# Kernel optimization log

Measured on AMD Instinct MI355X. Metric: run time of the kernel, lower is better.

Reference implementation:

```python
import jax, jax.numpy as jnp
import numpy as np

SIGMAS = [0.5, 1.0, 2.0, 4.0, 8.0]
FILTER_SIZE = int(4 * SIGMAS[-1] + 1)  # 33
PAD = int(2 * SIGMAS[-1])              # 16
K1, K2 = 0.01, 0.03
ALPHA = 0.025
COMPENSATION = 20.0
DATA_RANGE = 1.0


def _gauss_2d(size, sigma):
    coords = np.arange(size, dtype=np.float32) - size // 2
    g = np.exp(-coords ** 2 / (2.0 * sigma ** 2))
    g = g / g.sum()
    return np.outer(g, g)


def _build_g_masks():
    # [n_sigmas, 1, 33, 33] OIHW
    masks = np.stack([_gauss_2d(FILTER_SIZE, s)[None] for s in SIGMAS], axis=0)
    return jnp.asarray(masks, dtype=jnp.float32)


def setup_inputs() -> dict:
    key = jax.random.key(0)
    kx, ky = jax.random.split(key)
    x = jax.random.uniform(kx, (16, 1, 512, 512), dtype=jnp.float32)
    y = jax.random.uniform(ky, (16, 1, 512, 512), dtype=jnp.float32)
    return {"x": x, "y": y, "g_masks": _build_g_masks()}


def _conv(t, w):
    # t: [B,1,H,W], w: [O,1,33,33] -> [B,O,H,W] ('same' padding)
    return jax.lax.conv_general_dilated(
        t, w, window_strides=(1, 1), padding=[(PAD, PAD), (PAD, PAD)],
        dimension_numbers=("NCHW", "OIHW", "NCHW"))


def reference(x, y, g_masks):
    C1 = (K1 * DATA_RANGE) ** 2
    C2 = (K2 * DATA_RANGE) ** 2

    mux = _conv(x, g_masks)   # [B,5,H,W]
    muy = _conv(y, g_masks)
    mux2 = mux * mux
    muy2 = muy * muy
    muxy = mux * muy
    sigmax2 = _conv(x * x, g_masks) - mux2
    sigmay2 = _conv(y * y, g_masks) - muy2
    sigmaxy = _conv(x * y, g_masks) - muxy

    luminance = (2.0 * muxy + C1) / (mux2 + muy2 + C1)
    cs = (2.0 * sigmaxy + C2) / (sigmax2 + sigmay2 + C2)

    lM = luminance[:, -1, :, :]          # largest-scale luminance
    PIcs = jnp.prod(cs, axis=1)          # product of contrast-structure over scales
    loss_ms_ssim = 1.0 - lM * PIcs       # [B,H,W]

    loss_l1 = jnp.abs(x - y)             # [B,1,H,W]
    gaussian_l1 = _conv(loss_l1, g_masks[-1:]).mean(axis=1)  # [B,H,W]

    loss_mix = ALPHA * loss_ms_ssim + (1.0 - ALPHA) * gaussian_l1 / DATA_RANGE
    return (COMPENSATION * loss_mix).mean()
```

## Files before the change

kernel.cpp:

```cpp
#include <hip/hip_runtime.h>
#include <hip/hip_bf16.h>

namespace {

constexpr float kAlpha = 0.025f;
constexpr float kC1 = 1.0e-4f;
constexpr float kC2 = 9.0e-4f;

constexpr int MPS = 72;
constexpr int HTS = 72;

typedef __attribute__((ext_vector_type(8))) short short8;
typedef __attribute__((ext_vector_type(4))) float f32x4;

struct __align__(16) Smem {
  union {
    short mp[2][64 * MPS];
    short hbT[4][32 * HTS];
  };
  short l1T[32 * HTS];
  float red[4];
  int gtab[2][5][48];
};

union Frag {
  int i[4];
  int4 i4;
  short8 s8;
};

__device__ __forceinline__ unsigned f2bf(float f) {
  unsigned u = __float_as_uint(f);
  return (u + 0x7FFFu + ((u >> 16) & 1u)) >> 16;
}
__device__ __forceinline__ unsigned pk(float a, float b) {
  union {
    __hip_bfloat162 h;
    unsigned u;
  } c;
  c.h = __float22bfloat162_rn(make_float2(a, b));
  return c.u;
}
__device__ __forceinline__ float bfl(unsigned u) {
  return __uint_as_float(u << 16);
}
__device__ __forceinline__ float bfh(unsigned u) {
  return __uint_as_float(u & 0xFFFF0000u);
}
__device__ __forceinline__ float frcp(float x) {
  return __builtin_amdgcn_rcpf(x);
}

__device__ __forceinline__ short8 wbuild2(const int* tb, int nt, int kt) {
  Frag u;
#pragma unroll
  for (int j = 0; j < 4; ++j) u.i[j] = tb[16 * kt - 8 * nt + 8 + j];
  return u.s8;
}

__device__ __forceinline__ void load_xy(const Smem& sm, int row, int quad,
                                        Frag fx[2], Frag fy[2]) {
  const short* px = &sm.mp[0][row * MPS + quad * 8];
  const short* py = &sm.mp[1][row * MPS + quad * 8];
  fx[0].i4 = *(const int4*)(px);
  fx[1].i4 = *(const int4*)(px + 32);
  fy[0].i4 = *(const int4*)(py);
  fy[1].i4 = *(const int4*)(py + 32);
}

template <bool USE_WS>
__global__ __launch_bounds__(256, 4) void msssim_l1_kernel(
    const float* __restrict__ x, const float* __restrict__ y,
    const float* __restrict__ gm, float* __restrict__ partial,
    float* __restrict__ out) {
  __shared__ Smem sm;
  const int tid = threadIdx.x;
  const int lane = tid & 63;
  const int w = tid >> 6;
  const int quad = lane >> 4;
  const int l16 = lane & 15;
  const f32x4 kZ = {0.f, 0.f, 0.f, 0.f};

  float corr;
  {
    float traw4 = (lane < 33) ? gm[4 * 1089 + 528 + lane] : 0.f;
    float g = traw4 * rsqrtf(__shfl(traw4, 16, 64));
    float se = g, st = bfl(f2bf(g));
#pragma unroll
    for (int off = 32; off > 0; off >>= 1) {
      se += __shfl_xor(se, off, 64);
      st += __shfl_xor(st, off, 64);
    }
    float r1 = se / st;
    corr = r1 * r1;
  }

  {
    int* gt = &sm.gtab[0][0][0];
    for (int q = tid; q < 480; q += 256) {
      int par = q >= 240;
      int rem = par ? q - 240 : q;
      int s = rem / 48;
      int i = rem - s * 48;
      int t0 = 2 * i + par;
      const float* grow = gm + s * 1089 + 528;
      float rsc = rsqrtf(grow[16]);
      int g0 = t0 - 31, g1 = t0 - 30;
      unsigned lo = (g0 >= 0 && g0 <= 32) ? f2bf(grow[g0] * rsc) : 0u;
      unsigned hi = (g1 >= 0 && g1 <= 32) ? f2bf(grow[g1] * rsc) : 0u;
      gt[q] = (int)(lo | (hi << 16));
    }
  }

  const int D = (quad * 8 - l16 + 31) >> 1;
  const int* gD = &sm.gtab[(l16 & 1) ? 0 : 1][0][0] + D - 8;

  const float* xb = x + blockIdx.z * (512 * 512);
  const float* yb = y + blockIdx.z * (512 * 512);
  const int rb = blockIdx.y * 32 - 16;
  const int cb = blockIdx.x * 32 - 16;
  for (int f = tid; f < 1024; f += 256) {
    int pr = f >> 4;
    int pc = (f & 15) << 2;
    int gr = rb + pr, gc = cb + pc;
    float4 vx = make_float4(0.f, 0.f, 0.f, 0.f);
    float4 vy = vx;
    if (gr >= 0 && gr < 512 && gc >= 0 && gc < 512) {
      vx = *(const float4*)(xb + gr * 512 + gc);
      vy = *(const float4*)(yb + gr * 512 + gc);
    }
    const int base = pr * MPS + pc;
    *(int2*)(&sm.mp[0][base]) =
        make_int2((int)pk(vx.x, vx.y), (int)pk(vx.z, vx.w));
    *(int2*)(&sm.mp[1][base]) =
        make_int2((int)pk(vy.x, vy.y), (int)pk(vy.z, vy.w));
  }
  __syncthreads();

  Frag A[4][2];
  Frag dA[2];
#pragma unroll
  for (int mt = 0; mt < 4; ++mt) {
    Frag fx[2], fy[2];
    load_xy(sm, mt * 16 + l16, quad, fx, fy);
    if (mt == w) {
#pragma unroll
      for (int h = 0; h < 2; ++h)
#pragma unroll
        for (int i = 0; i < 4; ++i) {
          unsigned ux = (unsigned)fx[h].i[i], uy = (unsigned)fy[h].i[i];
          dA[h].i[i] =
              (int)pk(fabsf(bfl(ux) - bfl(uy)), fabsf(bfh(ux) - bfh(uy)));
        }
    }
    if (w == 0) {
      A[mt][0] = fx[0];
      A[mt][1] = fx[1];
    } else if (w == 1) {
      A[mt][0] = fy[0];
      A[mt][1] = fy[1];
    } else {
#pragma unroll
      for (int h = 0; h < 2; ++h)
#pragma unroll
        for (int i = 0; i < 4; ++i) {
          unsigned ux = (unsigned)fx[h].i[i], uy = (unsigned)fy[h].i[i];
          float xl = bfl(ux), xh = bfh(ux), yl = bfl(uy), yh = bfh(uy);
          A[mt][h].i[i] = (w == 2) ? (int)pk(fmaf(xl, xl, yl * yl),
                                            fmaf(xh, xh, yh * yh))
                                   : (int)pk(xl * yl, xh * yh);
        }
    }
  }

  {
    const int* tb = gD + 4 * 48;
#pragma unroll
    for (int nt = 0; nt < 2; ++nt) {
      short8 w0 = wbuild2(tb, nt, 0);
      short8 w1 = wbuild2(tb, nt, 1);
      f32x4 acc = __builtin_amdgcn_mfma_f32_16x16x32_bf16(dA[0].s8, w0, kZ, 0,
                                                          0, 0);
      acc = __builtin_amdgcn_mfma_f32_16x16x32_bf16(dA[1].s8, w1, acc, 0, 0,
                                                    0);
      *(int2*)(&sm.l1T[(nt * 16 + l16) * HTS + w * 16 + quad * 4]) =
          make_int2((int)pk(acc[0], acc[1]), (int)pk(acc[2], acc[3]));
    }
  }
  __syncthreads();

  const int mtv = w >> 1, ntv = w & 1;
  f32x4 Pcs = {1.f, 1.f, 1.f, 1.f};
  f32x4 lumP = {0.f, 0.f, 0.f, 0.f};
  f32x4 l1v = {0.f, 0.f, 0.f, 0.f};

#pragma unroll
  for (int s = 0; s < 5; ++s) {
    const int* tb = gD + s * 48;
#pragma unroll
    for (int nt = 0; nt < 2; ++nt) {
      short8 w0 = wbuild2(tb, nt, 0);
      short8 w1 = wbuild2(tb, nt, 1);
#pragma unroll
      for (int mt = 0; mt < 4; ++mt) {
        f32x4 acc = __builtin_amdgcn_mfma_f32_16x16x32_bf16(A[mt][0].s8, w0,
                                                            kZ, 0, 0, 0);
        acc = __builtin_amdgcn_mfma_f32_16x16x32_bf16(A[mt][1].s8, w1, acc, 0,
                                                      0, 0);
        *(int2*)(&sm.hbT[w][(nt * 16 + l16) * HTS + mt * 16 + quad * 4]) =
            make_int2((int)pk(acc[0], acc[1]), (int)pk(acc[2], acc[3]));
      }
    }
    __syncthreads();

    short8 wa0 = wbuild2(tb, mtv, 0);
    short8 wa1 = wbuild2(tb, mtv, 1);
    f32x4 mux, muy, T;
#pragma unroll
    for (int m = 0; m < 4; ++m) {
      const short* bp = &sm.hbT[m][(ntv * 16 + l16) * HTS + quad * 8];
      Frag b0, b1;
      b0.i4 = *(const int4*)(bp);
      b1.i4 = *(const int4*)(bp + 32);
      f32x4 acc =
          __builtin_amdgcn_mfma_f32_16x16x32_bf16(wa0, b0.s8, kZ, 0, 0, 0);
      acc = __builtin_amdgcn_mfma_f32_16x16x32_bf16(wa1, b1.s8, acc, 0, 0, 0);
      if (m == 0) {
        mux = acc;
      } else if (m == 1) {
        muy = acc;
      } else if (m == 2) {
#pragma unroll
        for (int r = 0; r < 4; ++r)
          T[r] = (acc[r] - mux[r] * mux[r]) - muy[r] * muy[r];
      } else {
#pragma unroll
        for (int r = 0; r < 4; ++r) {
          float cs =
              (2.f * (acc[r] - mux[r] * muy[r]) + kC2) * frcp(T[r] + kC2);
          Pcs[r] *= cs;
          if (s == 4)
            lumP[r] = ((2.f * (mux[r] * muy[r]) + kC1) *
                       frcp((mux[r] * mux[r] + muy[r] * muy[r]) + kC1)) *
                      Pcs[r];
        }
      }
    }
    if (s == 4) {
      const short* lp = &sm.l1T[(ntv * 16 + l16) * HTS + quad * 8];
      Frag c0, c1;
      c0.i4 = *(const int4*)(lp);
      c1.i4 = *(const int4*)(lp + 32);
      f32x4 a2 =
          __builtin_amdgcn_mfma_f32_16x16x32_bf16(wa0, c0.s8, kZ, 0, 0, 0);
      a2 = __builtin_amdgcn_mfma_f32_16x16x32_bf16(wa1, c1.s8, a2, 0, 0, 0);
#pragma unroll
      for (int r = 0; r < 4; ++r) l1v[r] = a2[r] * corr;
    }
    __syncthreads();
  }

  float lsum = 0.f;
#pragma unroll
  for (int r = 0; r < 4; ++r)
    lsum += kAlpha * (1.f - lumP[r]) + (1.f - kAlpha) * l1v[r];
#pragma unroll
  for (int off = 32; off > 0; off >>= 1) lsum += __shfl_down(lsum, off, 64);
  if ((tid & 63) == 0) sm.red[tid >> 6] = lsum;
  __syncthreads();
  if (tid == 0) {
    float t = sm.red[0] + sm.red[1] + sm.red[2] + sm.red[3];
    if (USE_WS) {
      partial[blockIdx.x + (blockIdx.y << 4) + (blockIdx.z << 8)] = t;
    } else {
      atomicAdd(out, t * (20.f / (16.f * 512.f * 512.f)));
    }
  }
}

__global__ __launch_bounds__(256) void msssim_reduce_kernel(
    const float* __restrict__ partial, float* __restrict__ out) {
  const int tid = threadIdx.x;
  float s = 0.f;
#pragma unroll
  for (int i = 0; i < 16; ++i) s += partial[tid + (i << 8)];
#pragma unroll
  for (int off = 32; off > 0; off >>= 1) s += __shfl_xor(s, off, 64);
  __shared__ float red[4];
  if ((tid & 63) == 0) red[tid >> 6] = s;
  __syncthreads();
  if (tid == 0)
    out[0] =
        (red[0] + red[1] + red[2] + red[3]) * (20.f / (16.f * 512.f * 512.f));
}

}

extern "C" void kernel_launch(void* const* d_in, const int* in_sizes, int n_in,
                              void* d_out, int out_size, void* d_ws,
                              size_t ws_size, hipStream_t stream) {
  (void)in_sizes;
  (void)n_in;
  (void)out_size;
  const float* x = (const float*)d_in[0];
  const float* y = (const float*)d_in[1];
  const float* gm = (const float*)d_in[2];
  float* out = (float*)d_out;
  dim3 grid(16, 16, 16);
  if (d_ws != nullptr && ws_size >= 4096 * sizeof(float)) {
    float* partial = (float*)d_ws;
    msssim_l1_kernel<true>
        <<<grid, dim3(256), 0, stream>>>(x, y, gm, partial, out);
    msssim_reduce_kernel<<<1, dim3(256), 0, stream>>>(partial, out);
  } else {
    hipMemsetAsync(out, 0, sizeof(float), stream);
    msssim_l1_kernel<false>
        <<<grid, dim3(256), 0, stream>>>(x, y, gm, nullptr, out);
  }
}
```

Measured before the change: 126.0 us.

## Precompute x²+y² and xy planes in shared memory during tile load

The tile load now computes x²+y² and x·y in fp32 from the global loads and stores them as two extra bf16 planes in shared memory. Each wave then loads its A operand straight from its own plane, with no per-wave branching or per-fragment recompute. The shared row stride changes from 72 to 66 shorts to keep the union size down and alter bank mapping, so the 16-byte reads become pairs of 8-byte reads. The shared footprint grows, which could lower occupancy. The product terms are now formed from fp32 inputs rather than bf16-rounded ones, which changes numerics slightly.

```diff
diff --git a/kernel.cpp b/kernel.cpp
--- a/kernel.cpp
+++ b/kernel.cpp
@@ -7,7 +7,7 @@
 constexpr float kC1 = 1.0e-4f;
 constexpr float kC2 = 9.0e-4f;
 
-constexpr int MPS = 72;
+constexpr int MPS = 66;
 constexpr int HTS = 72;
 
 typedef __attribute__((ext_vector_type(8))) short short8;
@@ -15,7 +15,7 @@
 
 struct __align__(16) Smem {
   union {
-    short mp[2][64 * MPS];
+    short mp[4][64 * MPS];
     short hbT[4][32 * HTS];
   };
   short l1T[32 * HTS];
@@ -56,16 +56,6 @@
 #pragma unroll
   for (int j = 0; j < 4; ++j) u.i[j] = tb[16 * kt - 8 * nt + 8 + j];
   return u.s8;
-}
-
-__device__ __forceinline__ void load_xy(const Smem& sm, int row, int quad,
-                                        Frag fx[2], Frag fy[2]) {
-  const short* px = &sm.mp[0][row * MPS + quad * 8];
-  const short* py = &sm.mp[1][row * MPS + quad * 8];
-  fx[0].i4 = *(const int4*)(px);
-  fx[1].i4 = *(const int4*)(px + 32);
-  fy[0].i4 = *(const int4*)(py);
-  fy[1].i4 = *(const int4*)(py + 32);
 }
 
 template <bool USE_WS>
@@ -134,6 +124,14 @@
         make_int2((int)pk(vx.x, vx.y), (int)pk(vx.z, vx.w));
     *(int2*)(&sm.mp[1][base]) =
         make_int2((int)pk(vy.x, vy.y), (int)pk(vy.z, vy.w));
+    float s0 = fmaf(vx.x, vx.x, vy.x * vy.x);
+    float s1 = fmaf(vx.y, vx.y, vy.y * vy.y);
+    float s2 = fmaf(vx.z, vx.z, vy.z * vy.z);
+    float s3 = fmaf(vx.w, vx.w, vy.w * vy.w);
+    *(int2*)(&sm.mp[2][base]) = make_int2((int)pk(s0, s1), (int)pk(s2, s3));
+    *(int2*)(&sm.mp[3][base]) =
+        make_int2((int)pk(vx.x * vy.x, vx.y * vy.y),
+                  (int)pk(vx.z * vy.z, vx.w * vy.w));
   }
   __syncthreads();
 
@@ -141,36 +139,33 @@
   Frag dA[2];
 #pragma unroll
   for (int mt = 0; mt < 4; ++mt) {
+    const short* pa = &sm.mp[w][(mt * 16 + l16) * MPS + quad * 8];
+    *(int2*)&A[mt][0].i[0] = *(const int2*)(pa);
+    *(int2*)&A[mt][0].i[2] = *(const int2*)(pa + 4);
+    *(int2*)&A[mt][1].i[0] = *(const int2*)(pa + 32);
+    *(int2*)&A[mt][1].i[2] = *(const int2*)(pa + 36);
+  }
+  {
+    const int row = (w * 16 + l16) * MPS + quad * 8;
+    const short* px = &sm.mp[0][row];
+    const short* py = &sm.mp[1][row];
     Frag fx[2], fy[2];
-    load_xy(sm, mt * 16 + l16, quad, fx, fy);
-    if (mt == w) {
-#pragma unroll
-      for (int h = 0; h < 2; ++h)
-#pragma unroll
-        for (int i = 0; i < 4; ++i) {
-          unsigned ux = (unsigned)fx[h].i[i], uy = (unsigned)fy[h].i[i];
-          dA[h].i[i] =
-              (int)pk(fabsf(bfl(ux) - bfl(uy)), fabsf(bfh(ux) - bfh(uy)));
-        }
-    }
-    if (w == 0) {
-      A[mt][0] = fx[0];
-      A[mt][1] = fx[1];
-    } else if (w == 1) {
-      A[mt][0] = fy[0];
-      A[mt][1] = fy[1];
-    } else {
-#pragma unroll
-      for (int h = 0; h < 2; ++h)
-#pragma unroll
-        for (int i = 0; i < 4; ++i) {
-          unsigned ux = (unsigned)fx[h].i[i], uy = (unsigned)fy[h].i[i];
-          float xl = bfl(ux), xh = bfh(ux), yl = bfl(uy), yh = bfh(uy);
-          A[mt][h].i[i] = (w == 2) ? (int)pk(fmaf(xl, xl, yl * yl),
-                                            fmaf(xh, xh, yh * yh))
-                                   : (int)pk(xl * yl, xh * yh);
-        }
-    }
+    *(int2*)&fx[0].i[0] = *(const int2*)(px);
+    *(int2*)&fx[0].i[2] = *(const int2*)(px + 4);
+    *(int2*)&fx[1].i[0] = *(const int2*)(px + 32);
+    *(int2*)&fx[1].i[2] = *(const int2*)(px + 36);
+    *(int2*)&fy[0].i[0] = *(const int2*)(py);
+    *(int2*)&fy[0].i[2] = *(const int2*)(py + 4);
+    *(int2*)&fy[1].i[0] = *(const int2*)(py + 32);
+    *(int2*)&fy[1].i[2] = *(const int2*)(py + 36);
+#pragma unroll
+    for (int h = 0; h < 2; ++h)
+#pragma unroll
+      for (int i = 0; i < 4; ++i) {
+        unsigned ux = (unsigned)fx[h].i[i], uy = (unsigned)fy[h].i[i];
+        dA[h].i[i] =
+            (int)pk(fabsf(bfl(ux) - bfl(uy)), fabsf(bfh(ux) - bfh(uy)));
+      }
   }
 
   {
```

After: 164.4 us. +30.5%, slower.
